# Optimization experiments

Measured on AMD Instinct MI355X. Metric: run time of the kernel, lower is better.

The kernel has to match this reference:

```python
import jax, jax.numpy as jnp
import numpy as np
from jax import lax

TAU = 1.0
LAMBDA_CONTRAST = 1.0
GAMMA_ALIGN = 1.0
EPSILON = 0.1
SINKHORN_ITERS = 50
B, V_EN, V_CN, K, H, D = 512, 30000, 20000, 100, 512, 300


def setup_inputs() -> dict:
    key = jax.random.key(0)
    ks = jax.random.split(key, 24)
    s = lambda fan_in: 1.0 / np.sqrt(fan_in)
    inp = {
        'x_bow_en': jax.random.uniform(ks[0], (B, V_EN), jnp.float32),
        'x_bow_cn': jax.random.uniform(ks[1], (B, V_CN), jnp.float32),
        'cluster_ids': jax.random.randint(ks[2], (B,), 0, 9, jnp.int32),
        'eps_en': jax.random.normal(ks[3], (B, K), jnp.float32),
        'eps_cn': jax.random.normal(ks[4], (B, K), jnp.float32),
        # English encoder params
        'W1_en': jax.random.normal(ks[5], (V_EN, H), jnp.float32) * s(V_EN),
        'b1_en': jnp.zeros((H,), jnp.float32),
        'W2_en': jax.random.normal(ks[6], (H, H), jnp.float32) * s(H),
        'b2_en': jnp.zeros((H,), jnp.float32),
        'Wmu_en': jax.random.normal(ks[7], (H, K), jnp.float32) * s(H),
        'bmu_en': jnp.zeros((K,), jnp.float32),
        'Wlv_en': jax.random.normal(ks[8], (H, K), jnp.float32) * s(H),
        'blv_en': jnp.zeros((K,), jnp.float32),
        # Chinese encoder params
        'W1_cn': jax.random.normal(ks[9], (V_CN, H), jnp.float32) * s(V_CN),
        'b1_cn': jnp.zeros((H,), jnp.float32),
        'W2_cn': jax.random.normal(ks[10], (H, H), jnp.float32) * s(H),
        'b2_cn': jnp.zeros((H,), jnp.float32),
        'Wmu_cn': jax.random.normal(ks[11], (H, K), jnp.float32) * s(H),
        'bmu_cn': jnp.zeros((K,), jnp.float32),
        'Wlv_cn': jax.random.normal(ks[12], (H, K), jnp.float32) * s(H),
        'blv_cn': jnp.zeros((K,), jnp.float32),
        # frozen word embeddings + topic embeddings
        'word_emb_en': jax.random.normal(ks[13], (V_EN, D), jnp.float32),
        'word_emb_cn': jax.random.normal(ks[14], (V_CN, D), jnp.float32),
        'topic_emb': jax.random.normal(ks[15], (K, D), jnp.float32),
    }
    return inp


def _encoder(x, eps, W1, b1, W2, b2, Wmu, bmu, Wlv, blv):
    h = jax.nn.softplus(x @ W1 + b1)
    h = jax.nn.softplus(h @ W2 + b2)
    mu = h @ Wmu + bmu
    logvar = h @ Wlv + blv
    z = mu + eps * jnp.exp(0.5 * logvar)  # reparameterization
    theta = jax.nn.softmax(z, axis=-1)
    return theta, mu, logvar


def _compute_beta(word_emb, topic_emb, tau):
    # torch.cdist p=2 -> euclidean distance [V, K]
    sq = (jnp.sum(word_emb ** 2, -1)[:, None] + jnp.sum(topic_emb ** 2, -1)[None, :]
          - 2.0 * word_emb @ topic_emb.T)
    dist = jnp.sqrt(jnp.maximum(sq, 0.0))
    beta = jnp.exp(-dist / tau)
    beta = beta / jnp.sum(beta, axis=0, keepdims=True)  # normalize over vocab
    return beta.T  # [K, V]


def _tm_loss(x_bow, theta, beta, mu, logvar):
    recon = theta @ beta  # [B, V]
    recon_loss = jnp.mean(-jnp.sum(x_bow * jax.nn.log_softmax(recon, axis=-1), axis=-1))
    kl = jnp.mean(0.5 * jnp.sum(jnp.exp(logvar) + mu ** 2 - 1.0 - logvar, axis=-1))
    return recon_loss + kl


def _contrastive_loss(theta_en, theta_cn, cluster_ids, tau):
    b = theta_en.shape[0]
    parity = (jnp.arange(b) % 2 == 0)[:, None]
    thetas = jnp.where(parity, theta_en, theta_cn)  # anchor/other selection
    tn = thetas / jnp.maximum(jnp.linalg.norm(thetas, axis=-1, keepdims=True), 1e-8)
    E = jnp.exp((tn @ tn.T) / tau)  # exp(cos_sim / tau), [B, B]
    offdiag = ~jnp.eye(b, dtype=bool)
    valid = cluster_ids > 0  # falsy cluster -> skipped, matching torch truthiness
    same = cluster_ids[:, None] == cluster_ids[None, :]
    pos_mask = offdiag & same & valid[:, None] & valid[None, :]
    pos_sim = jnp.sum(jnp.where(pos_mask, E, 0.0), axis=1)
    neg_sum = jnp.sum(jnp.where(offdiag, E, 0.0), axis=1)  # all j != i
    has_pos = valid & (jnp.sum(pos_mask, axis=1) > 0)
    per = -jnp.log(pos_sim / (pos_sim + neg_sum + 1e-8))
    loss = jnp.sum(jnp.where(has_pos, per, 0.0))
    count = jnp.sum(has_pos).astype(jnp.float32)
    return loss / (count + 1e-8)


def _sinkhorn(a, b, C, eps):
    Kmat = jnp.exp(-C / eps)
    def step(uv, _):
        u, v = uv
        u = a / (Kmat @ v + 1e-8)
        v = b / (Kmat.T @ u + 1e-8)
        return (u, v), None
    (u, v), _ = lax.scan(step, (jnp.ones_like(a), jnp.ones_like(b)), None, length=SINKHORN_ITERS)
    return u[:, None] * Kmat * v[None, :]


def _alignment_loss(topic_emb, eps):
    tn = topic_emb / jnp.maximum(jnp.linalg.norm(topic_emb, axis=-1, keepdims=True), 1e-8)
    C = 1.0 - tn @ tn.T
    k = topic_emb.shape[0]
    a = jnp.full((k,), 1.0 / k, jnp.float32)
    Q = _sinkhorn(a, a, C, eps)
    return jnp.sum(Q * C)


def reference(x_bow_en, x_bow_cn, cluster_ids, eps_en, eps_cn,
              W1_en, b1_en, W2_en, b2_en, Wmu_en, bmu_en, Wlv_en, blv_en,
              W1_cn, b1_cn, W2_cn, b2_cn, Wmu_cn, bmu_cn, Wlv_cn, blv_cn,
              word_emb_en, word_emb_cn, topic_emb):
    theta_en, mu_en, lv_en = _encoder(x_bow_en, eps_en, W1_en, b1_en, W2_en, b2_en, Wmu_en, bmu_en, Wlv_en, blv_en)
    theta_cn, mu_cn, lv_cn = _encoder(x_bow_cn, eps_cn, W1_cn, b1_cn, W2_cn, b2_cn, Wmu_cn, bmu_cn, Wlv_cn, blv_cn)
    beta_en = _compute_beta(word_emb_en, topic_emb, TAU)
    beta_cn = _compute_beta(word_emb_cn, topic_emb, TAU)
    tm_en = _tm_loss(x_bow_en, theta_en, beta_en, mu_en, lv_en)
    tm_cn = _tm_loss(x_bow_cn, theta_cn, beta_cn, mu_cn, lv_cn)
    contrast = _contrastive_loss(theta_en, theta_cn, cluster_ids, TAU)
    align = _alignment_loss(topic_emb, EPSILON)
    total = tm_en + tm_cn + LAMBDA_CONTRAST * contrast + GAMMA_ALIGN * align
    return total, tm_en, tm_cn, contrast, align, theta_en, theta_cn, beta_en, beta_cn
```

## Files before the change

kernel.cpp:

```cpp
#include <hip/hip_runtime.h>
#include <math.h>

#define BATCH 512
#define VEN 30000
#define VCN 20000
#define KT 100
#define HID 512
#define DIM 300
#define VENP 30080
#define VCNP 20096
#define KDP 320
#define VENK 30080
#define VCNK 20096

typedef float f32x4 __attribute__((ext_vector_type(4)));
typedef short bf16x8 __attribute__((ext_vector_type(8)));
typedef unsigned short u16x8 __attribute__((ext_vector_type(8)));
typedef unsigned int u32;

#define WS_H1_EN   0
#define WS_H2_EN   (WS_H1_EN + 262144)
#define WS_H1_CN   (WS_H2_EN + 262144)
#define WS_H2_CN   (WS_H1_CN + 262144)
#define WS_ROWS_EN (WS_H2_CN + 262144)
#define WS_ROWS_CN (WS_ROWS_EN + 1536)
#define WS_SCAL    (WS_ROWS_CN + 1536)
#define ZERO_FLOATS (WS_SCAL + 64)
#define WS_BIG     ZERO_FLOATS
#define XB_EN      WS_BIG
#define XB_CN      (WS_BIG + 7700480)
#define WEP_EN     WS_BIG
#define WEP_CN     (WS_BIG + 4812800)
#define TEP        (WS_BIG + 4812800 + 3215360)
#define BT_EN      (WS_BIG + 8048640)
#define BT_CN      (BT_EN + 1925120)
#define THP_EN     (BT_CN + 1286144)
#define THP_CN     (THP_EN + 32768)
#define AFTER_BIG  (WS_BIG + 12845056)
#define W1T_EN     AFTER_BIG
#define W1T_CN     (W1T_EN + 7700480)
#define W2T_EN     (W1T_CN + 5144576)
#define W2T_CN     (W2T_EN + 131072)
#define H1B_EN     (W2T_CN + 131072)
#define H1B_CN     (H1B_EN + 131072)
#define WN2_EN     (H1B_CN + 131072)
#define WN2_CN     (WN2_EN + 30080)
#define TN2        (WN2_CN + 20096)
#define WS_TNBUF   (TN2 + 128)
#define WS_TNT     (WS_TNBUF + 51200)
#define WS_CTOP    (WS_TNT + 30000)
#define WS_COLSUM_EN (WS_CTOP + 10000)
#define WS_COLSUM_CN (WS_COLSUM_EN + 128)

#define OUT_THETA_EN 5
#define OUT_THETA_CN (OUT_THETA_EN + 51200)
#define OUT_BETA_EN  (OUT_THETA_CN + 51200)
#define OUT_BETA_CN  (OUT_BETA_EN + 3000000)

__device__ __forceinline__ float waveReduceSum(float v) {
    #pragma unroll
    for (int o = 32; o > 0; o >>= 1) v += __shfl_down(v, o);
    return v;
}

__device__ __forceinline__ unsigned short f2bf(float f) {
    unsigned int u = __float_as_uint(f);
    u = (u + 0x7FFFu + ((u >> 16) & 1u)) >> 16;
    return (unsigned short)u;
}

__device__ __forceinline__ void gl2lds16(const unsigned short* g, unsigned short* l) {
    __builtin_amdgcn_global_load_lds(
        (const __attribute__((address_space(1))) u32*)g,
        (__attribute__((address_space(3))) u32*)l, 16, 0, 0);
}

__global__ __launch_bounds__(256)
void cast_pad_bf16_kernel(const float* __restrict__ src, unsigned short* __restrict__ dst,
                          int cols, int colsPad)
{
    int row = blockIdx.y;
    int col = (blockIdx.x * 256 + threadIdx.x) * 8;
    if (col >= colsPad) return;
    u16x8 o = {0,0,0,0,0,0,0,0};
    if (col < cols) {
        float4 a = *(const float4*)&src[(size_t)row * cols + col];
        float4 b = *(const float4*)&src[(size_t)row * cols + col + 4];
        o = (u16x8){ f2bf(a.x), f2bf(a.y), f2bf(a.z), f2bf(a.w),
                     f2bf(b.x), f2bf(b.y), f2bf(b.z), f2bf(b.w) };
    }
    *(u16x8*)&dst[(size_t)row * colsPad + col] = o;
}

__global__ __launch_bounds__(256)
void gemm1_async(const unsigned short* __restrict__ A, const unsigned short* __restrict__ B,
                 float* __restrict__ C, int N, int ldA, int ldB, int chunkK, int K)
{
    __shared__ __align__(16) unsigned short As[128 * 64];
    __shared__ __align__(16) unsigned short Bs[128 * 64];
    const int tid = threadIdx.x;
    const int m0 = blockIdx.x * 128, n0 = blockIdx.y * 128;
    const int kStart = blockIdx.z * chunkK;
    const int kEnd = min(kStart + chunkK, K);

    const int wave = tid >> 6, lane = tid & 63;
    const int wm = (wave & 1) * 64, wn = (wave >> 1) * 64;
    const int l15 = lane & 15, quad = lane >> 4;

    const int rl = lane >> 3;
    const int cs = (lane & 7) ^ rl;

    f32x4 acc[4][4];
    #pragma unroll
    for (int i = 0; i < 4; ++i)
        #pragma unroll
        for (int j = 0; j < 4; ++j)
            acc[i][j] = (f32x4){0.f, 0.f, 0.f, 0.f};

    for (int k0 = kStart; k0 < kEnd; k0 += 64) {
        #pragma unroll
        for (int j = 0; j < 4; ++j) {
            int seg = wave * 4 + j;
            int r = seg * 8 + rl;
            gl2lds16(A + (size_t)(m0 + r) * ldA + k0 + cs * 8, &As[seg * 512]);
            gl2lds16(B + (size_t)(n0 + r) * ldB + k0 + cs * 8, &Bs[seg * 512]);
        }
        asm volatile("s_waitcnt vmcnt(0)" ::: "memory");
        __syncthreads();

        #pragma unroll
        for (int kh = 0; kh < 2; ++kh) {
            bf16x8 af[4], bfr[4];
            #pragma unroll
            for (int mi = 0; mi < 4; ++mi) {
                int r = wm + mi * 16 + l15;
                af[mi] = *(const bf16x8*)&As[r * 64 + (((kh << 2) | quad) ^ (r & 7)) * 8];
            }
            #pragma unroll
            for (int ni = 0; ni < 4; ++ni) {
                int r = wn + ni * 16 + l15;
                bfr[ni] = *(const bf16x8*)&Bs[r * 64 + (((kh << 2) | quad) ^ (r & 7)) * 8];
            }
            #pragma unroll
            for (int mi = 0; mi < 4; ++mi)
                #pragma unroll
                for (int ni = 0; ni < 4; ++ni)
                    acc[mi][ni] = __builtin_amdgcn_mfma_f32_16x16x32_bf16(af[mi], bfr[ni], acc[mi][ni], 0, 0, 0);
        }
        __syncthreads();
    }

    #pragma unroll
    for (int mi = 0; mi < 4; ++mi)
        #pragma unroll
        for (int ni = 0; ni < 4; ++ni)
            #pragma unroll
            for (int i = 0; i < 4; ++i) {
                int m = m0 + wm + mi * 16 + quad * 4 + i;
                int n = n0 + wn + ni * 16 + l15;
                atomicAdd(&C[(size_t)m * N + n], acc[mi][ni][i]);
            }
}

template <int MODE, int AF32>
__global__ __launch_bounds__(256)
void mfma_gemm_nt(const void* __restrict__ Av, const unsigned short* __restrict__ B,
                  float* __restrict__ C, int M, int N, int K, int ldA, int ldB, int chunkK,
                  int Mreal, const float* __restrict__ an2, const float* __restrict__ bn2)
{
    __shared__ __align__(16) unsigned short As[128 * 40];
    __shared__ __align__(16) unsigned short Bs[128 * 40];
    const int tid = threadIdx.x;
    const int m0 = blockIdx.x * 128, n0 = blockIdx.y * 128;
    const int kStart = blockIdx.z * chunkK;
    const int kEnd = min(kStart + chunkK, K);

    const int wave = tid >> 6, lane = tid & 63;
    const int wm = (wave & 1) * 64, wn = (wave >> 1) * 64;
    const int l15 = lane & 15, quad = lane >> 4;

    const int srow = tid >> 1;
    const int scol = (tid & 1) * 16;

    f32x4 acc[4][4];
    #pragma unroll
    for (int i = 0; i < 4; ++i)
        #pragma unroll
        for (int j = 0; j < 4; ++j)
            acc[i][j] = (f32x4){0.f, 0.f, 0.f, 0.f};

    const u16x8 z8 = {0,0,0,0,0,0,0,0};

    for (int k0 = kStart; k0 < kEnd; k0 += 32) {
        int kA = k0 + scol;
        if (AF32) {
            const float* pa = (const float*)Av + (size_t)(m0 + srow) * ldA + kA;
            float4 f0 = {0,0,0,0}, f1 = {0,0,0,0}, f2 = {0,0,0,0}, f3 = {0,0,0,0};
            if (kA < kEnd) {
                f0 = *(const float4*)(pa);
                f1 = *(const float4*)(pa + 4);
                f2 = *(const float4*)(pa + 8);
                f3 = *(const float4*)(pa + 12);
            }
            u16x8 o0 = { f2bf(f0.x), f2bf(f0.y), f2bf(f0.z), f2bf(f0.w),
                         f2bf(f1.x), f2bf(f1.y), f2bf(f1.z), f2bf(f1.w) };
            u16x8 o1 = { f2bf(f2.x), f2bf(f2.y), f2bf(f2.z), f2bf(f2.w),
                         f2bf(f3.x), f2bf(f3.y), f2bf(f3.z), f2bf(f3.w) };
            *(u16x8*)&As[srow * 40 + scol]     = o0;
            *(u16x8*)&As[srow * 40 + scol + 8] = o1;
        } else {
            const unsigned short* pa = (const unsigned short*)Av + (size_t)(m0 + srow) * ldA + kA;
            u16x8 a0 = (kA     < kEnd) ? *(const u16x8*)(pa)     : z8;
            u16x8 a1 = (kA + 8 < kEnd) ? *(const u16x8*)(pa + 8) : z8;
            *(u16x8*)&As[srow * 40 + scol]     = a0;
            *(u16x8*)&As[srow * 40 + scol + 8] = a1;
        }
        {
            const unsigned short* pb = B + (size_t)(n0 + srow) * ldB + kA;
            u16x8 b0 = (kA     < kEnd) ? *(const u16x8*)(pb)     : z8;
            u16x8 b1 = (kA + 8 < kEnd) ? *(const u16x8*)(pb + 8) : z8;
            *(u16x8*)&Bs[srow * 40 + scol]     = b0;
            *(u16x8*)&Bs[srow * 40 + scol + 8] = b1;
        }
        __syncthreads();
        bf16x8 af[4], bfr[4];
        #pragma unroll
        for (int mi = 0; mi < 4; ++mi)
            af[mi] = *(const bf16x8*)&As[(wm + mi * 16 + l15) * 40 + quad * 8];
        #pragma unroll
        for (int ni = 0; ni < 4; ++ni)
            bfr[ni] = *(const bf16x8*)&Bs[(wn + ni * 16 + l15) * 40 + quad * 8];
        #pragma unroll
        for (int mi = 0; mi < 4; ++mi)
            #pragma unroll
            for (int ni = 0; ni < 4; ++ni)
                acc[mi][ni] = __builtin_amdgcn_mfma_f32_16x16x32_bf16(af[mi], bfr[ni], acc[mi][ni], 0, 0, 0);
        __syncthreads();
    }

    if (MODE == 0) {
        #pragma unroll
        for (int mi = 0; mi < 4; ++mi)
            #pragma unroll
            for (int ni = 0; ni < 4; ++ni)
                #pragma unroll
                for (int i = 0; i < 4; ++i) {
                    int m = m0 + wm + mi * 16 + quad * 4 + i;
                    int n = n0 + wn + ni * 16 + l15;
                    atomicAdd(&C[(size_t)m * N + n], acc[mi][ni][i]);
                }
    } else {
        #pragma unroll
        for (int mi = 0; mi < 4; ++mi)
            #pragma unroll
            for (int ni = 0; ni < 4; ++ni)
                #pragma unroll
                for (int i = 0; i < 4; ++i) {
                    int m = m0 + wm + mi * 16 + quad * 4 + i;
                    int n = n0 + wn + ni * 16 + l15;
                    if (m < Mreal && n < KT) {
                        float sq = an2[m] + bn2[n] - 2.f * acc[mi][ni][i];
                        C[(size_t)n * Mreal + m] = __expf(-sqrtf(fmaxf(sq, 0.f)));
                    }
                }
    }
}

__global__ __launch_bounds__(256)
void recon_mfma_kernel(const unsigned short* __restrict__ A, const unsigned short* __restrict__ B,
                       const float* __restrict__ x, int V, float* __restrict__ rows)
{
    __shared__ __align__(16) unsigned short As[128 * 40];
    __shared__ __align__(16) unsigned short Bs[128 * 40];
    const int tid = threadIdx.x;
    const int m0 = blockIdx.x * 128, n0 = blockIdx.y * 128;
    const int wave = tid >> 6, lane = tid & 63;
    const int wm = (wave & 1) * 64, wn = (wave >> 1) * 64;
    const int l15 = lane & 15, quad = lane >> 4;
    const int srow = tid >> 1, scol = (tid & 1) * 16;

    f32x4 acc[4][4];
    #pragma unroll
    for (int i = 0; i < 4; ++i)
        #pragma unroll
        for (int j = 0; j < 4; ++j)
            acc[i][j] = (f32x4){0.f, 0.f, 0.f, 0.f};

    for (int k0 = 0; k0 < 128; k0 += 32) {
        int kA = k0 + scol;
        *(u16x8*)&As[srow * 40 + scol]     = *(const u16x8*)(A + (size_t)(m0 + srow) * 128 + kA);
        *(u16x8*)&As[srow * 40 + scol + 8] = *(const u16x8*)(A + (size_t)(m0 + srow) * 128 + kA + 8);
        *(u16x8*)&Bs[srow * 40 + scol]     = *(const u16x8*)(B + (size_t)(n0 + srow) * 128 + kA);
        *(u16x8*)&Bs[srow * 40 + scol + 8] = *(const u16x8*)(B + (size_t)(n0 + srow) * 128 + kA + 8);
        __syncthreads();
        bf16x8 af[4], bfr[4];
        #pragma unroll
        for (int mi = 0; mi < 4; ++mi)
            af[mi] = *(const bf16x8*)&As[(wm + mi * 16 + l15) * 40 + quad * 8];
        #pragma unroll
        for (int ni = 0; ni < 4; ++ni)
            bfr[ni] = *(const bf16x8*)&Bs[(wn + ni * 16 + l15) * 40 + quad * 8];
        #pragma unroll
        for (int mi = 0; mi < 4; ++mi)
            #pragma unroll
            for (int ni = 0; ni < 4; ++ni)
                acc[mi][ni] = __builtin_amdgcn_mfma_f32_16x16x32_bf16(af[mi], bfr[ni], acc[mi][ni], 0, 0, 0);
        __syncthreads();
    }

    #pragma unroll
    for (int ni = 0; ni < 4; ++ni) {
        int b = n0 + wn + ni * 16 + l15;
        float tse = 0.f, tsxr = 0.f, tsx = 0.f;
        #pragma unroll
        for (int mi = 0; mi < 4; ++mi) {
            int v0 = m0 + wm + mi * 16 + quad * 4;
            if (v0 + 3 < V) {
                float4 xv = *(const float4*)&x[(size_t)b * V + v0];
                float xa[4] = {xv.x, xv.y, xv.z, xv.w};
                #pragma unroll
                for (int i = 0; i < 4; ++i) {
                    float r = acc[mi][ni][i];
                    tse += __expf(r);
                    tsxr += xa[i] * r;
                    tsx  += xa[i];
                }
            } else {
                #pragma unroll
                for (int i = 0; i < 4; ++i) {
                    int v = v0 + i;
                    if (v < V) {
                        float xv1 = x[(size_t)b * V + v];
                        float r = acc[mi][ni][i];
                        tse += __expf(r); tsxr += xv1 * r; tsx += xv1;
                    }
                }
            }
        }
        tse  += __shfl_xor(tse, 16);  tse  += __shfl_xor(tse, 32);
        tsxr += __shfl_xor(tsxr, 16); tsxr += __shfl_xor(tsxr, 32);
        tsx  += __shfl_xor(tsx, 16);  tsx  += __shfl_xor(tsx, 32);
        if (quad == 0) {
            atomicAdd(&rows[b], tse);
            atomicAdd(&rows[512 + b], tsxr);
            atomicAdd(&rows[1024 + b], tsx);
        }
    }
}

__global__ __launch_bounds__(256)
void transpose_cast_kernel(const float* __restrict__ src, unsigned short* __restrict__ dst,
                           int K, int N, int Kp)
{
    __shared__ float tile[32][33];
    int kb = blockIdx.x * 32, nb = blockIdx.y * 32;
    int tx = threadIdx.x & 31, ty4 = threadIdx.x >> 5;
    #pragma unroll
    for (int j = 0; j < 4; ++j) {
        int k = kb + ty4 * 4 + j;
        tile[ty4 * 4 + j][tx] = (k < K) ? src[(size_t)k * N + nb + tx] : 0.f;
    }
    __syncthreads();
    #pragma unroll
    for (int j = 0; j < 4; ++j) {
        int n = nb + ty4 * 4 + j;
        int k = kb + tx;
        if (k < Kp) dst[(size_t)n * Kp + k] = f2bf(tile[tx][ty4 * 4 + j]);
    }
}

__global__ void padcast_sqnorm_kernel(const float* __restrict__ src, unsigned short* __restrict__ dst,
                                      float* __restrict__ n2, int V)
{
    int m = blockIdx.x, tid = threadIdx.x;
    float sq = 0.f;
    #pragma unroll
    for (int j = 0; j < 5; ++j) {
        int k = tid + j * 64;
        float v = (m < V && k < DIM) ? src[(size_t)m * DIM + k] : 0.f;
        dst[(size_t)m * KDP + k] = f2bf(v);
        sq += v * v;
    }
    sq = waveReduceSum(sq);
    if (tid == 0) n2[m] = sq;
}

__global__ __launch_bounds__(256)
void normbeta_bt_kernel(float* __restrict__ beta, const float* __restrict__ cs,
                        unsigned short* __restrict__ bt, int V)
{
    int v = blockIdx.x * 64 + (threadIdx.x & 63);
    int kq = threadIdx.x >> 6;
    unsigned short tmp[32];
    #pragma unroll
    for (int j = 0; j < 32; ++j) {
        int k = kq * 32 + j;
        float val = 0.f;
        if (k < KT && v < V) {
            val = beta[(size_t)k * V + v] * (1.0f / cs[k]);
            beta[(size_t)k * V + v] = val;
        }
        tmp[j] = f2bf(val);
    }
    #pragma unroll
    for (int q = 0; q < 4; ++q)
        *(u16x8*)&bt[(size_t)v * 128 + kq * 32 + q * 8] = *(u16x8*)&tmp[q * 8];
}

__global__ void theta_pad_kernel(const float* __restrict__ theta, unsigned short* __restrict__ thp)
{
    int idx = blockIdx.x * 256 + threadIdx.x;
    int b = idx >> 7, k = idx & 127;
    thp[idx] = f2bf(k < KT ? theta[b * KT + k] : 0.f);
}

__global__ __launch_bounds__(256)
void colsum_kernel(const float* __restrict__ bta, float* __restrict__ cs, int V)
{
    int k = blockIdx.x, tid = threadIdx.x;
    float s = 0.f;
    for (int v = tid; v < V; v += 256) s += bta[(size_t)k * V + v];
    s = waveReduceSum(s);
    __shared__ float cw[4];
    if ((tid & 63) == 0) cw[tid >> 6] = s;
    __syncthreads();
    if (tid == 0) cs[k] = cw[0] + cw[1] + cw[2] + cw[3];
}

__global__ void bias_softplus_bf16_kernel(const float* __restrict__ src, const float* __restrict__ b,
                                          unsigned short* __restrict__ dst, int n)
{
    int i = blockIdx.x * 256 + threadIdx.x;
    if (i < n) {
        float x = src[i] + b[i & (HID - 1)];
        float sp = fmaxf(x, 0.f) + log1pf(__expf(-fabsf(x)));
        dst[i] = f2bf(sp);
    }
}

__global__ void bias_softplus_f32_kernel(float* __restrict__ y, const float* __restrict__ b, int n)
{
    int i = blockIdx.x * 256 + threadIdx.x;
    if (i < n) {
        float x = y[i] + b[i & (HID - 1)];
        y[i] = fmaxf(x, 0.f) + log1pf(__expf(-fabsf(x)));
    }
}

__global__ __launch_bounds__(128)
void encoder_head_kernel(const float* __restrict__ h2, const float* __restrict__ Wmu,
                         const float* __restrict__ bmu, const float* __restrict__ Wlv,
                         const float* __restrict__ blv, const float* __restrict__ eps,
                         float* __restrict__ theta_out, float* __restrict__ kl_accum)
{
    int i = blockIdx.x, tid = threadIdx.x;
    __shared__ float hrow[HID];
    __shared__ float sred[128];
    #pragma unroll
    for (int j = 0; j < 4; ++j) hrow[tid + 128 * j] = h2[i * HID + tid + 128 * j];
    __syncthreads();
    float mu = 0.f, lv = 0.f;
    if (tid < KT) {
        #pragma unroll 8
        for (int h = 0; h < HID; ++h) {
            float hv = hrow[h];
            mu += hv * Wmu[h * KT + tid];
            lv += hv * Wlv[h * KT + tid];
        }
        mu += bmu[tid]; lv += blv[tid];
    }
    float z = (tid < KT) ? (mu + eps[i * KT + tid] * __expf(0.5f * lv)) : -3.0e38f;
    sred[tid] = z; __syncthreads();
    for (int s = 64; s > 0; s >>= 1) { if (tid < s) sred[tid] = fmaxf(sred[tid], sred[tid + s]); __syncthreads(); }
    float zmax = sred[0]; __syncthreads();
    float e = (tid < KT) ? __expf(z - zmax) : 0.f;
    sred[tid] = e; __syncthreads();
    for (int s = 64; s > 0; s >>= 1) { if (tid < s) sred[tid] += sred[tid + s]; __syncthreads(); }
    float esum = sred[0]; __syncthreads();
    if (tid < KT) theta_out[i * KT + tid] = e / esum;
    float kterm = (tid < KT) ? 0.5f * (__expf(lv) + mu * mu - 1.f - lv) : 0.f;
    sred[tid] = kterm; __syncthreads();
    for (int s = 64; s > 0; s >>= 1) { if (tid < s) sred[tid] += sred[tid + s]; __syncthreads(); }
    if (tid == 0) atomicAdd(kl_accum, sred[0]);
}

__global__ __launch_bounds__(256)
void recon_finalize_kernel(const float* __restrict__ rows_en, const float* __restrict__ rows_cn,
                           float* __restrict__ scal)
{
    const float* rows = (blockIdx.x == 0) ? rows_en : rows_cn;
    int tid = threadIdx.x;
    float s = 0.f;
    for (int r = tid; r < 512; r += 256) {
        float se = rows[r], sxr = rows[512 + r], sx = rows[1024 + r];
        s += __logf(se) * sx - sxr;
    }
    s = waveReduceSum(s);
    __shared__ float cw[4];
    if ((tid & 63) == 0) cw[tid >> 6] = s;
    __syncthreads();
    if (tid == 0) scal[5 + blockIdx.x] = cw[0] + cw[1] + cw[2] + cw[3];
}

__global__ __launch_bounds__(128)
void contrast_prep_kernel(const float* __restrict__ theta_en, const float* __restrict__ theta_cn,
                          float* __restrict__ tn)
{
    int i = blockIdx.x, tid = threadIdx.x;
    const float* src = ((i & 1) == 0) ? theta_en : theta_cn;
    float val = (tid < KT) ? src[i * KT + tid] : 0.f;
    __shared__ float sred[128];
    sred[tid] = val * val; __syncthreads();
    for (int s = 64; s > 0; s >>= 1) { if (tid < s) sred[tid] += sred[tid + s]; __syncthreads(); }
    float inv = 1.0f / fmaxf(sqrtf(sred[0]), 1e-8f);
    if (tid < KT) tn[i * KT + tid] = val * inv;
}

__global__ __launch_bounds__(256)
void contrast_main_kernel(const float* __restrict__ tn, const int* __restrict__ cid,
                          float* __restrict__ scal)
{
    int i = blockIdx.x, tid = threadIdx.x;
    __shared__ __align__(16) float ti[KT];
    if (tid < KT) ti[tid] = tn[i * KT + tid];
    __syncthreads();
    int ci = cid[i];
    bool vi = ci > 0;
    float pos = 0.f, neg = 0.f, pcnt = 0.f;
    for (int j = tid; j < 512; j += 256) {
        if (j == i) continue;
        float s = 0.f;
        const float4* tj = reinterpret_cast<const float4*>(&tn[j * KT]);
        #pragma unroll
        for (int q = 0; q < 25; ++q) {
            float4 t4 = tj[q];
            s += ti[4 * q] * t4.x + ti[4 * q + 1] * t4.y + ti[4 * q + 2] * t4.z + ti[4 * q + 3] * t4.w;
        }
        float E = __expf(s);
        neg += E;
        if (vi && cid[j] == ci) { pos += E; pcnt += 1.f; }
    }
    pos = waveReduceSum(pos); neg = waveReduceSum(neg); pcnt = waveReduceSum(pcnt);
    __shared__ float cw[3][4];
    int w = tid >> 6;
    if ((tid & 63) == 0) { cw[0][w] = pos; cw[1][w] = neg; cw[2][w] = pcnt; }
    __syncthreads();
    if (tid == 0) {
        float P = 0.f, N = 0.f, PC = 0.f;
        for (int q = 0; q < 4; ++q) { P += cw[0][q]; N += cw[1][q]; PC += cw[2][q]; }
        if (vi && PC > 0.f) {
            atomicAdd(&scal[2], -__logf(P / (P + N + 1e-8f)));
            atomicAdd(&scal[3], 1.0f);
        }
    }
}

__global__ void norm_rows_kernel(const float* __restrict__ A, float* __restrict__ out, int cols)
{
    int r = blockIdx.x, tid = threadIdx.x;
    float s = 0.f;
    for (int d = tid; d < cols; d += 64) { float a = A[r * cols + d]; s += a * a; }
    s = waveReduceSum(s);
    s = __shfl(s, 0);
    float inv = 1.0f / fmaxf(sqrtf(s), 1e-8f);
    for (int d = tid; d < cols; d += 64) out[r * cols + d] = A[r * cols + d] * inv;
}

__global__ __launch_bounds__(128)
void ctopic_kernel(const float* __restrict__ tnt, float* __restrict__ C)
{
    int i = blockIdx.x, tid = threadIdx.x;
    __shared__ float ti[DIM];
    for (int d = tid; d < DIM; d += 128) ti[d] = tnt[i * DIM + d];
    __syncthreads();
    for (int j = tid; j < KT; j += 128) {
        float s = 0.f;
        for (int d = 0; d < DIM; ++d) s += ti[d] * tnt[j * DIM + d];
        C[i * KT + j] = 1.0f - s;
    }
}

__global__ __launch_bounds__(128, 1)
void sinkhorn_kernel(const float* __restrict__ C, float* __restrict__ scal)
{
    __shared__ __align__(16) float ld[100 * 101];
    __shared__ __align__(16) float ub[128], vb[128];
    __shared__ float cw[2];
    const int tid = threadIdx.x;

    for (int i = tid; i < 10000; i += 128) {
        int r = i / 100, c = i - r * 100;
        ld[r * 101 + c] = C[i];
    }
    ub[tid] = 1.f; vb[tid] = 1.f;
    __syncthreads();

    float kr[100], kc[100];
    if (tid < 100) {
        #pragma unroll
        for (int j = 0; j < 100; ++j) kr[j] = __expf(-10.f * ld[tid * 101 + j]);
        #pragma unroll
        for (int j = 0; j < 100; ++j) kc[j] = __expf(-10.f * ld[j * 101 + tid]);
    }

    for (int it = 0; it < 50; ++it) {
        if (tid < 100) {
            float s = 0.f;
            #pragma unroll
            for (int q = 0; q < 25; ++q) {
                float4 v4 = *(const float4*)&vb[q * 4];
                s += kr[q*4]*v4.x + kr[q*4+1]*v4.y + kr[q*4+2]*v4.z + kr[q*4+3]*v4.w;
            }
            ub[tid] = 0.01f / (s + 1e-8f);
        }
        __syncthreads();
        if (tid < 100) {
            float s = 0.f;
            #pragma unroll
            for (int q = 0; q < 25; ++q) {
                float4 u4 = *(const float4*)&ub[q * 4];
                s += kc[q*4]*u4.x + kc[q*4+1]*u4.y + kc[q*4+2]*u4.z + kc[q*4+3]*u4.w;
            }
            vb[tid] = 0.01f / (s + 1e-8f);
        }
        __syncthreads();
    }

    float part = 0.f;
    if (tid < 100) {
        float u = ub[tid];
        #pragma unroll
        for (int q = 0; q < 25; ++q) {
            float4 v4 = *(const float4*)&vb[q * 4];
            float va[4] = {v4.x, v4.y, v4.z, v4.w};
            #pragma unroll
            for (int e = 0; e < 4; ++e) {
                int j = q * 4 + e;
                part += u * kr[j] * va[e] * ld[tid * 101 + j];
            }
        }
    }
    part = waveReduceSum(part);
    if ((tid & 63) == 0) cw[tid >> 6] = part;
    __syncthreads();
    if (tid == 0) scal[4] = cw[0] + cw[1];
}

__global__ void final_combine_kernel(const float* __restrict__ scal, float* __restrict__ out)
{
    if (threadIdx.x == 0 && blockIdx.x == 0) {
        const float invB = 1.0f / 512.0f;
        float tm_en = scal[5] * invB + scal[0] * invB;
        float tm_cn = scal[6] * invB + scal[1] * invB;
        float contrast = scal[2] / (scal[3] + 1e-8f);
        float align = scal[4];
        out[0] = tm_en + tm_cn + contrast + align;
        out[1] = tm_en;
        out[2] = tm_cn;
        out[3] = contrast;
        out[4] = align;
    }
}

extern "C" void kernel_launch(void* const* d_in, const int* in_sizes, int n_in,
                              void* d_out_v, int out_size, void* d_ws, size_t ws_size,
                              hipStream_t stream)
{
    const float* x_en   = (const float*)d_in[0];
    const float* x_cn   = (const float*)d_in[1];
    const int*   cid    = (const int*)  d_in[2];
    const float* eps_en = (const float*)d_in[3];
    const float* eps_cn = (const float*)d_in[4];
    const float* W1_en  = (const float*)d_in[5];
    const float* b1_en  = (const float*)d_in[6];
    const float* W2_en  = (const float*)d_in[7];
    const float* b2_en  = (const float*)d_in[8];
    const float* Wmu_en = (const float*)d_in[9];
    const float* bmu_en = (const float*)d_in[10];
    const float* Wlv_en = (const float*)d_in[11];
    const float* blv_en = (const float*)d_in[12];
    const float* W1_cn  = (const float*)d_in[13];
    const float* b1_cn  = (const float*)d_in[14];
    const float* W2_cn  = (const float*)d_in[15];
    const float* b2_cn  = (const float*)d_in[16];
    const float* Wmu_cn = (const float*)d_in[17];
    const float* bmu_cn = (const float*)d_in[18];
    const float* Wlv_cn = (const float*)d_in[19];
    const float* blv_cn = (const float*)d_in[20];
    const float* we_en  = (const float*)d_in[21];
    const float* we_cn  = (const float*)d_in[22];
    const float* te     = (const float*)d_in[23];
    float* out = (float*)d_out_v;
    float* ws  = (float*)d_ws;

    unsigned short* w1t_en = (unsigned short*)(ws + W1T_EN);
    unsigned short* w1t_cn = (unsigned short*)(ws + W1T_CN);
    unsigned short* w2t_en = (unsigned short*)(ws + W2T_EN);
    unsigned short* w2t_cn = (unsigned short*)(ws + W2T_CN);
    unsigned short* h1b_en = (unsigned short*)(ws + H1B_EN);
    unsigned short* h1b_cn = (unsigned short*)(ws + H1B_CN);
    unsigned short* xb_en  = (unsigned short*)(ws + XB_EN);
    unsigned short* xb_cn  = (unsigned short*)(ws + XB_CN);
    unsigned short* wep_en = (unsigned short*)(ws + WEP_EN);
    unsigned short* wep_cn = (unsigned short*)(ws + WEP_CN);
    unsigned short* tep    = (unsigned short*)(ws + TEP);
    unsigned short* bt_en  = (unsigned short*)(ws + BT_EN);
    unsigned short* bt_cn  = (unsigned short*)(ws + BT_CN);
    unsigned short* thp_en = (unsigned short*)(ws + THP_EN);
    unsigned short* thp_cn = (unsigned short*)(ws + THP_CN);

    hipMemsetAsync(d_ws, 0, (size_t)ZERO_FLOATS * sizeof(float), stream);

    cast_pad_bf16_kernel<<<dim3(15, 512), 256, 0, stream>>>(x_en, xb_en, VEN, VENK);
    cast_pad_bf16_kernel<<<dim3(10, 512), 256, 0, stream>>>(x_cn, xb_cn, VCN, VCNK);

    transpose_cast_kernel<<<dim3(940, 16), 256, 0, stream>>>(W1_en, w1t_en, VEN, HID, VENK);
    transpose_cast_kernel<<<dim3(628, 16), 256, 0, stream>>>(W1_cn, w1t_cn, VCN, HID, VCNK);
    transpose_cast_kernel<<<dim3(16, 16), 256, 0, stream>>>(W2_en, w2t_en, HID, HID, HID);
    transpose_cast_kernel<<<dim3(16, 16), 256, 0, stream>>>(W2_cn, w2t_cn, HID, HID, HID);

    gemm1_async<<<dim3(4, 4, 47), 256, 0, stream>>>(xb_en, w1t_en, ws + WS_H1_EN,
        HID, VENK, VENK, 640, VENK);
    gemm1_async<<<dim3(4, 4, 32), 256, 0, stream>>>(xb_cn, w1t_cn, ws + WS_H1_CN,
        HID, VCNK, VCNK, 640, VCNK);

    bias_softplus_bf16_kernel<<<1024, 256, 0, stream>>>(ws + WS_H1_EN, b1_en, h1b_en, 262144);
    bias_softplus_bf16_kernel<<<1024, 256, 0, stream>>>(ws + WS_H1_CN, b1_cn, h1b_cn, 262144);

    mfma_gemm_nt<0, 0><<<dim3(4, 4, 16), 256, 0, stream>>>(h1b_en, w2t_en, ws + WS_H2_EN,
        BATCH, HID, HID, HID, HID, 32, 0, nullptr, nullptr);
    mfma_gemm_nt<0, 0><<<dim3(4, 4, 16), 256, 0, stream>>>(h1b_cn, w2t_cn, ws + WS_H2_CN,
        BATCH, HID, HID, HID, HID, 32, 0, nullptr, nullptr);

    bias_softplus_f32_kernel<<<1024, 256, 0, stream>>>(ws + WS_H2_EN, b2_en, 262144);
    bias_softplus_f32_kernel<<<1024, 256, 0, stream>>>(ws + WS_H2_CN, b2_cn, 262144);

    encoder_head_kernel<<<BATCH, 128, 0, stream>>>(ws + WS_H2_EN, Wmu_en, bmu_en, Wlv_en, blv_en,
                                                   eps_en, out + OUT_THETA_EN, ws + WS_SCAL + 0);
    encoder_head_kernel<<<BATCH, 128, 0, stream>>>(ws + WS_H2_CN, Wmu_cn, bmu_cn, Wlv_cn, blv_cn,
                                                   eps_cn, out + OUT_THETA_CN, ws + WS_SCAL + 1);

    padcast_sqnorm_kernel<<<VENP, 64, 0, stream>>>(we_en, wep_en, ws + WN2_EN, VEN);
    padcast_sqnorm_kernel<<<VCNP, 64, 0, stream>>>(we_cn, wep_cn, ws + WN2_CN, VCN);
    padcast_sqnorm_kernel<<<128, 64, 0, stream>>>(te, tep, ws + TN2, KT);

    mfma_gemm_nt<2, 0><<<dim3(235, 1, 1), 256, 0, stream>>>(wep_en, tep, out + OUT_BETA_EN,
        VENP, 128, KDP, KDP, KDP, KDP, VEN, ws + WN2_EN, ws + TN2);
    mfma_gemm_nt<2, 0><<<dim3(157, 1, 1), 256, 0, stream>>>(wep_cn, tep, out + OUT_BETA_CN,
        VCNP, 128, KDP, KDP, KDP, KDP, VCN, ws + WN2_CN, ws + TN2);

    colsum_kernel<<<KT, 256, 0, stream>>>(out + OUT_BETA_EN, ws + WS_COLSUM_EN, VEN);
    colsum_kernel<<<KT, 256, 0, stream>>>(out + OUT_BETA_CN, ws + WS_COLSUM_CN, VCN);

    normbeta_bt_kernel<<<VENP / 64, 256, 0, stream>>>(out + OUT_BETA_EN, ws + WS_COLSUM_EN, bt_en, VEN);
    normbeta_bt_kernel<<<VCNP / 64, 256, 0, stream>>>(out + OUT_BETA_CN, ws + WS_COLSUM_CN, bt_cn, VCN);

    theta_pad_kernel<<<256, 256, 0, stream>>>(out + OUT_THETA_EN, thp_en);
    theta_pad_kernel<<<256, 256, 0, stream>>>(out + OUT_THETA_CN, thp_cn);

    recon_mfma_kernel<<<dim3(VENP / 128, 4), 256, 0, stream>>>(bt_en, thp_en, x_en, VEN, ws + WS_ROWS_EN);
    recon_mfma_kernel<<<dim3(VCNP / 128, 4), 256, 0, stream>>>(bt_cn, thp_cn, x_cn, VCN, ws + WS_ROWS_CN);
    recon_finalize_kernel<<<2, 256, 0, stream>>>(ws + WS_ROWS_EN, ws + WS_ROWS_CN, ws + WS_SCAL);

    contrast_prep_kernel<<<BATCH, 128, 0, stream>>>(out + OUT_THETA_EN, out + OUT_THETA_CN, ws + WS_TNBUF);
    contrast_main_kernel<<<BATCH, 256, 0, stream>>>(ws + WS_TNBUF, cid, ws + WS_SCAL);

    norm_rows_kernel<<<KT, 64, 0, stream>>>(te, ws + WS_TNT, DIM);
    ctopic_kernel<<<KT, 128, 0, stream>>>(ws + WS_TNT, ws + WS_CTOP);
    sinkhorn_kernel<<<1, 128, 0, stream>>>(ws + WS_CTOP, ws + WS_SCAL);

    final_combine_kernel<<<1, 64, 0, stream>>>(ws + WS_SCAL, out);
}
```

Measured before the change: 891.2 us.

## Unify GEMMs on async LDS loader, drop split-K for layer 2, split Sinkhorn threads

```diff
diff --git a/kernel.cpp b/kernel.cpp
--- a/kernel.cpp
+++ b/kernel.cpp
@@ -92,9 +92,11 @@
     *(u16x8*)&dst[(size_t)row * colsPad + col] = o;
 }
 
-__global__ __launch_bounds__(256)
-void gemm1_async(const unsigned short* __restrict__ A, const unsigned short* __restrict__ B,
-                 float* __restrict__ C, int N, int ldA, int ldB, int chunkK, int K)
+template <int MODE>
+__global__ __launch_bounds__(256)
+void gemm_async(const unsigned short* __restrict__ A, const unsigned short* __restrict__ B,
+                float* __restrict__ C, int N, int ldA, int ldB, int chunkK, int K,
+                int Mreal, const float* __restrict__ an2, const float* __restrict__ bn2)
 {
     __shared__ __align__(16) unsigned short As[128 * 64];
     __shared__ __align__(16) unsigned short Bs[128 * 64];
@@ -158,126 +160,32 @@
             for (int i = 0; i < 4; ++i) {
                 int m = m0 + wm + mi * 16 + quad * 4 + i;
                 int n = n0 + wn + ni * 16 + l15;
-                atomicAdd(&C[(size_t)m * N + n], acc[mi][ni][i]);
-            }
-}
-
-template <int MODE, int AF32>
-__global__ __launch_bounds__(256)
-void mfma_gemm_nt(const void* __restrict__ Av, const unsigned short* __restrict__ B,
-                  float* __restrict__ C, int M, int N, int K, int ldA, int ldB, int chunkK,
-                  int Mreal, const float* __restrict__ an2, const float* __restrict__ bn2)
-{
-    __shared__ __align__(16) unsigned short As[128 * 40];
-    __shared__ __align__(16) unsigned short Bs[128 * 40];
-    const int tid = threadIdx.x;
-    const int m0 = blockIdx.x * 128, n0 = blockIdx.y * 128;
-    const int kStart = blockIdx.z * chunkK;
-    const int kEnd = min(kStart + chunkK, K);
-
-    const int wave = tid >> 6, lane = tid & 63;
-    const int wm = (wave & 1) * 64, wn = (wave >> 1) * 64;
-    const int l15 = lane & 15, quad = lane >> 4;
-
-    const int srow = tid >> 1;
-    const int scol = (tid & 1) * 16;
-
-    f32x4 acc[4][4];
-    #pragma unroll
-    for (int i = 0; i < 4; ++i)
-        #pragma unroll
-        for (int j = 0; j < 4; ++j)
-            acc[i][j] = (f32x4){0.f, 0.f, 0.f, 0.f};
-
-    const u16x8 z8 = {0,0,0,0,0,0,0,0};
-
-    for (int k0 = kStart; k0 < kEnd; k0 += 32) {
-        int kA = k0 + scol;
-        if (AF32) {
-            const float* pa = (const float*)Av + (size_t)(m0 + srow) * ldA + kA;
-            float4 f0 = {0,0,0,0}, f1 = {0,0,0,0}, f2 = {0,0,0,0}, f3 = {0,0,0,0};
-            if (kA < kEnd) {
-                f0 = *(const float4*)(pa);
-                f1 = *(const float4*)(pa + 4);
-                f2 = *(const float4*)(pa + 8);
-                f3 = *(const float4*)(pa + 12);
-            }
-            u16x8 o0 = { f2bf(f0.x), f2bf(f0.y), f2bf(f0.z), f2bf(f0.w),
-                         f2bf(f1.x), f2bf(f1.y), f2bf(f1.z), f2bf(f1.w) };
-            u16x8 o1 = { f2bf(f2.x), f2bf(f2.y), f2bf(f2.z), f2bf(f2.w),
-                         f2bf(f3.x), f2bf(f3.y), f2bf(f3.z), f2bf(f3.w) };
-            *(u16x8*)&As[srow * 40 + scol]     = o0;
-            *(u16x8*)&As[srow * 40 + scol + 8] = o1;
-        } else {
-            const unsigned short* pa = (const unsigned short*)Av + (size_t)(m0 + srow) * ldA + kA;
-            u16x8 a0 = (kA     < kEnd) ? *(const u16x8*)(pa)     : z8;
-            u16x8 a1 = (kA + 8 < kEnd) ? *(const u16x8*)(pa + 8) : z8;
-            *(u16x8*)&As[srow * 40 + scol]     = a0;
-            *(u16x8*)&As[srow * 40 + scol + 8] = a1;
-        }
-        {
-            const unsigned short* pb = B + (size_t)(n0 + srow) * ldB + kA;
-            u16x8 b0 = (kA     < kEnd) ? *(const u16x8*)(pb)     : z8;
-            u16x8 b1 = (kA + 8 < kEnd) ? *(const u16x8*)(pb + 8) : z8;
-            *(u16x8*)&Bs[srow * 40 + scol]     = b0;
-            *(u16x8*)&Bs[srow * 40 + scol + 8] = b1;
-        }
-        __syncthreads();
-        bf16x8 af[4], bfr[4];
-        #pragma unroll
-        for (int mi = 0; mi < 4; ++mi)
-            af[mi] = *(const bf16x8*)&As[(wm + mi * 16 + l15) * 40 + quad * 8];
-        #pragma unroll
-        for (int ni = 0; ni < 4; ++ni)
-            bfr[ni] = *(const bf16x8*)&Bs[(wn + ni * 16 + l15) * 40 + quad * 8];
-        #pragma unroll
-        for (int mi = 0; mi < 4; ++mi)
-            #pragma unroll
-            for (int ni = 0; ni < 4; ++ni)
-                acc[mi][ni] = __builtin_amdgcn_mfma_f32_16x16x32_bf16(af[mi], bfr[ni], acc[mi][ni], 0, 0, 0);
-        __syncthreads();
-    }
-
-    if (MODE == 0) {
-        #pragma unroll
-        for (int mi = 0; mi < 4; ++mi)
-            #pragma unroll
-            for (int ni = 0; ni < 4; ++ni)
-                #pragma unroll
-                for (int i = 0; i < 4; ++i) {
-                    int m = m0 + wm + mi * 16 + quad * 4 + i;
-                    int n = n0 + wn + ni * 16 + l15;
+                if (MODE == 0) {
                     atomicAdd(&C[(size_t)m * N + n], acc[mi][ni][i]);
-                }
-    } else {
-        #pragma unroll
-        for (int mi = 0; mi < 4; ++mi)
-            #pragma unroll
-            for (int ni = 0; ni < 4; ++ni)
-                #pragma unroll
-                for (int i = 0; i < 4; ++i) {
-                    int m = m0 + wm + mi * 16 + quad * 4 + i;
-                    int n = n0 + wn + ni * 16 + l15;
+                } else if (MODE == 1) {
+                    C[(size_t)m * N + n] = acc[mi][ni][i];
+                } else {
                     if (m < Mreal && n < KT) {
                         float sq = an2[m] + bn2[n] - 2.f * acc[mi][ni][i];
                         C[(size_t)n * Mreal + m] = __expf(-sqrtf(fmaxf(sq, 0.f)));
                     }
                 }
-    }
+            }
 }
 
 __global__ __launch_bounds__(256)
 void recon_mfma_kernel(const unsigned short* __restrict__ A, const unsigned short* __restrict__ B,
                        const float* __restrict__ x, int V, float* __restrict__ rows)
 {
-    __shared__ __align__(16) unsigned short As[128 * 40];
-    __shared__ __align__(16) unsigned short Bs[128 * 40];
+    __shared__ __align__(16) unsigned short As[128 * 64];
+    __shared__ __align__(16) unsigned short Bs[128 * 64];
     const int tid = threadIdx.x;
     const int m0 = blockIdx.x * 128, n0 = blockIdx.y * 128;
     const int wave = tid >> 6, lane = tid & 63;
     const int wm = (wave & 1) * 64, wn = (wave >> 1) * 64;
     const int l15 = lane & 15, quad = lane >> 4;
-    const int srow = tid >> 1, scol = (tid & 1) * 16;
+    const int rl = lane >> 3;
+    const int cs = (lane & 7) ^ rl;
 
     f32x4 acc[4][4];
     #pragma unroll
@@ -286,25 +194,36 @@
         for (int j = 0; j < 4; ++j)
             acc[i][j] = (f32x4){0.f, 0.f, 0.f, 0.f};
 
-    for (int k0 = 0; k0 < 128; k0 += 32) {
-        int kA = k0 + scol;
-        *(u16x8*)&As[srow * 40 + scol]     = *(const u16x8*)(A + (size_t)(m0 + srow) * 128 + kA);
-        *(u16x8*)&As[srow * 40 + scol + 8] = *(const u16x8*)(A + (size_t)(m0 + srow) * 128 + kA + 8);
-        *(u16x8*)&Bs[srow * 40 + scol]     = *(const u16x8*)(B + (size_t)(n0 + srow) * 128 + kA);
-        *(u16x8*)&Bs[srow * 40 + scol + 8] = *(const u16x8*)(B + (size_t)(n0 + srow) * 128 + kA + 8);
+    for (int k0 = 0; k0 < 128; k0 += 64) {
+        #pragma unroll
+        for (int j = 0; j < 4; ++j) {
+            int seg = wave * 4 + j;
+            int r = seg * 8 + rl;
+            gl2lds16(A + (size_t)(m0 + r) * 128 + k0 + cs * 8, &As[seg * 512]);
+            gl2lds16(B + (size_t)(n0 + r) * 128 + k0 + cs * 8, &Bs[seg * 512]);
+        }
+        asm volatile("s_waitcnt vmcnt(0)" ::: "memory");
         __syncthreads();
-        bf16x8 af[4], bfr[4];
-        #pragma unroll
-        for (int mi = 0; mi < 4; ++mi)
-            af[mi] = *(const bf16x8*)&As[(wm + mi * 16 + l15) * 40 + quad * 8];
-        #pragma unroll
-        for (int ni = 0; ni < 4; ++ni)
-            bfr[ni] = *(const bf16x8*)&Bs[(wn + ni * 16 + l15) * 40 + quad * 8];
-        #pragma unroll
-        for (int mi = 0; mi < 4; ++mi)
-            #pragma unroll
-            for (int ni = 0; ni < 4; ++ni)
-                acc[mi][ni] = __builtin_amdgcn_mfma_f32_16x16x32_bf16(af[mi], bfr[ni], acc[mi][ni], 0, 0, 0);
+
+        #pragma unroll
+        for (int kh = 0; kh < 2; ++kh) {
+            bf16x8 af[4], bfr[4];
+            #pragma unroll
+            for (int mi = 0; mi < 4; ++mi) {
+                int r = wm + mi * 16 + l15;
+                af[mi] = *(const bf16x8*)&As[r * 64 + (((kh << 2) | quad) ^ (r & 7)) * 8];
+            }
+            #pragma unroll
+            for (int ni = 0; ni < 4; ++ni) {
+                int r = wn + ni * 16 + l15;
+                bfr[ni] = *(const bf16x8*)&Bs[r * 64 + (((kh << 2) | quad) ^ (r & 7)) * 8];
+            }
+            #pragma unroll
+            for (int mi = 0; mi < 4; ++mi)
+                #pragma unroll
+                for (int ni = 0; ni < 4; ++ni)
+                    acc[mi][ni] = __builtin_amdgcn_mfma_f32_16x16x32_bf16(af[mi], bfr[ni], acc[mi][ni], 0, 0, 0);
+        }
         __syncthreads();
     }
 
@@ -580,70 +499,63 @@
     }
 }
 
-__global__ __launch_bounds__(128, 1)
+__global__ __launch_bounds__(256, 1)
 void sinkhorn_kernel(const float* __restrict__ C, float* __restrict__ scal)
 {
-    __shared__ __align__(16) float ld[100 * 101];
     __shared__ __align__(16) float ub[128], vb[128];
-    __shared__ float cw[2];
+    __shared__ float cw[4];
     const int tid = threadIdx.x;
-
-    for (int i = tid; i < 10000; i += 128) {
-        int r = i / 100, c = i - r * 100;
-        ld[r * 101 + c] = C[i];
-    }
-    ub[tid] = 1.f; vb[tid] = 1.f;
-    __syncthreads();
-
-    float kr[100], kc[100];
-    if (tid < 100) {
-        #pragma unroll
-        for (int j = 0; j < 100; ++j) kr[j] = __expf(-10.f * ld[tid * 101 + j]);
-        #pragma unroll
-        for (int j = 0; j < 100; ++j) kc[j] = __expf(-10.f * ld[j * 101 + tid]);
-    }
+    const bool gA = (tid < 100);
+    const bool gB = (tid >= 128 && tid < 228);
+    const int rc = gA ? tid : (tid - 128);
+
+    float kk[100];
+    if (gA) {
+        #pragma unroll
+        for (int j = 0; j < 100; ++j) kk[j] = __expf(-10.f * C[rc * 100 + j]);
+    } else if (gB) {
+        #pragma unroll
+        for (int j = 0; j < 100; ++j) kk[j] = __expf(-10.f * C[j * 100 + rc]);
+    }
+    if (tid < 128) { ub[tid] = 1.f; vb[tid] = 1.f; }
+    __syncthreads();
 
     for (int it = 0; it < 50; ++it) {
-        if (tid < 100) {
+        if (gA) {
             float s = 0.f;
             #pragma unroll
             for (int q = 0; q < 25; ++q) {
                 float4 v4 = *(const float4*)&vb[q * 4];
-                s += kr[q*4]*v4.x + kr[q*4+1]*v4.y + kr[q*4+2]*v4.z + kr[q*4+3]*v4.w;
-            }
-            ub[tid] = 0.01f / (s + 1e-8f);
+                s += kk[q*4]*v4.x + kk[q*4+1]*v4.y + kk[q*4+2]*v4.z + kk[q*4+3]*v4.w;
+            }
+            ub[rc] = 0.01f / (s + 1e-8f);
         }
         __syncthreads();
-        if (tid < 100) {
+        if (gB) {
             float s = 0.f;
             #pragma unroll
             for (int q = 0; q < 25; ++q) {
                 float4 u4 = *(const float4*)&ub[q * 4];
-                s += kc[q*4]*u4.x + kc[q*4+1]*u4.y + kc[q*4+2]*u4.z + kc[q*4+3]*u4.w;
-            }
-            vb[tid] = 0.01f / (s + 1e-8f);
+                s += kk[q*4]*u4.x + kk[q*4+1]*u4.y + kk[q*4+2]*u4.z + kk[q*4+3]*u4.w;
+            }
+            vb[rc] = 0.01f / (s + 1e-8f);
         }
         __syncthreads();
     }
 
     float part = 0.f;
-    if (tid < 100) {
-        float u = ub[tid];
-        #pragma unroll
-        for (int q = 0; q < 25; ++q) {
-            float4 v4 = *(const float4*)&vb[q * 4];
-            float va[4] = {v4.x, v4.y, v4.z, v4.w};
-            #pragma unroll
-            for (int e = 0; e < 4; ++e) {
-                int j = q * 4 + e;
-                part += u * kr[j] * va[e] * ld[tid * 101 + j];
-            }
+    if (gA) {
+        float u = ub[rc];
+        #pragma unroll
+        for (int j = 0; j < 100; ++j) {
+            float k = kk[j];
+            part += u * k * vb[j] * (-0.1f * __logf(k));
         }
     }
     part = waveReduceSum(part);
     if ((tid & 63) == 0) cw[tid >> 6] = part;
     __syncthreads();
-    if (tid == 0) scal[4] = cw[0] + cw[1];
+    if (tid == 0) scal[4] = cw[0] + cw[1] + cw[2] + cw[3];
 }
 
 __global__ void final_combine_kernel(const float* __restrict__ scal, float* __restrict__ out)
@@ -719,18 +631,18 @@
     transpose_cast_kernel<<<dim3(16, 16), 256, 0, stream>>>(W2_en, w2t_en, HID, HID, HID);
     transpose_cast_kernel<<<dim3(16, 16), 256, 0, stream>>>(W2_cn, w2t_cn, HID, HID, HID);
 
-    gemm1_async<<<dim3(4, 4, 47), 256, 0, stream>>>(xb_en, w1t_en, ws + WS_H1_EN,
-        HID, VENK, VENK, 640, VENK);
-    gemm1_async<<<dim3(4, 4, 32), 256, 0, stream>>>(xb_cn, w1t_cn, ws + WS_H1_CN,
-        HID, VCNK, VCNK, 640, VCNK);
+    gemm_async<0><<<dim3(4, 4, 47), 256, 0, stream>>>(xb_en, w1t_en, ws + WS_H1_EN,
+        HID, VENK, VENK, 640, VENK, 0, nullptr, nullptr);
+    gemm_async<0><<<dim3(4, 4, 32), 256, 0, stream>>>(xb_cn, w1t_cn, ws + WS_H1_CN,
+        HID, VCNK, VCNK, 640, VCNK, 0, nullptr, nullptr);
 
     bias_softplus_bf16_kernel<<<1024, 256, 0, stream>>>(ws + WS_H1_EN, b1_en, h1b_en, 262144);
     bias_softplus_bf16_kernel<<<1024, 256, 0, stream>>>(ws + WS_H1_CN, b1_cn, h1b_cn, 262144);
 
-    mfma_gemm_nt<0, 0><<<dim3(4, 4, 16), 256, 0, stream>>>(h1b_en, w2t_en, ws + WS_H2_EN,
-        BATCH, HID, HID, HID, HID, 32, 0, nullptr, nullptr);
-    mfma_gemm_nt<0, 0><<<dim3(4, 4, 16), 256, 0, stream>>>(h1b_cn, w2t_cn, ws + WS_H2_CN,
-        BATCH, HID, HID, HID, HID, 32, 0, nullptr, nullptr);
+    gemm_async<1><<<dim3(4, 4, 1), 256, 0, stream>>>(h1b_en, w2t_en, ws + WS_H2_EN,
+        HID, HID, HID, HID, HID, 0, nullptr, nullptr);
+    gemm_async<1><<<dim3(4, 4, 1), 256, 0, stream>>>(h1b_cn, w2t_cn, ws + WS_H2_CN,
+        HID, HID, HID, HID, HID, 0, nullptr, nullptr);
 
     bias_softplus_f32_kernel<<<1024, 256, 0, stream>>>(ws + WS_H2_EN, b2_en, 262144);
     bias_softplus_f32_kernel<<<1024, 256, 0, stream>>>(ws + WS_H2_CN, b2_cn, 262144);
@@ -744,10 +656,10 @@
     padcast_sqnorm_kernel<<<VCNP, 64, 0, stream>>>(we_cn, wep_cn, ws + WN2_CN, VCN);
     padcast_sqnorm_kernel<<<128, 64, 0, stream>>>(te, tep, ws + TN2, KT);
 
-    mfma_gemm_nt<2, 0><<<dim3(235, 1, 1), 256, 0, stream>>>(wep_en, tep, out + OUT_BETA_EN,
-        VENP, 128, KDP, KDP, KDP, KDP, VEN, ws + WN2_EN, ws + TN2);
-    mfma_gemm_nt<2, 0><<<dim3(157, 1, 1), 256, 0, stream>>>(wep_cn, tep, out + OUT_BETA_CN,
-        VCNP, 128, KDP, KDP, KDP, KDP, VCN, ws + WN2_CN, ws + TN2);
+    gemm_async<2><<<dim3(235, 1, 1), 256, 0, stream>>>(wep_en, tep, out + OUT_BETA_EN,
+        128, KDP, KDP, KDP, KDP, VEN, ws + WN2_EN, ws + TN2);
+    gemm_async<2><<<dim3(157, 1, 1), 256, 0, stream>>>(wep_cn, tep, out + OUT_BETA_CN,
+        128, KDP, KDP, KDP, KDP, VCN, ws + WN2_CN, ws + TN2);
 
     colsum_kernel<<<KT, 256, 0, stream>>>(out + OUT_BETA_EN, ws + WS_COLSUM_EN, VEN);
     colsum_kernel<<<KT, 256, 0, stream>>>(out + OUT_BETA_CN, ws + WS_COLSUM_CN, VCN);
@@ -767,7 +679,7 @@
 
     norm_rows_kernel<<<KT, 64, 0, stream>>>(te, ws + WS_TNT, DIM);
     ctopic_kernel<<<KT, 128, 0, stream>>>(ws + WS_TNT, ws + WS_CTOP);
-    sinkhorn_kernel<<<1, 128, 0, stream>>>(ws + WS_CTOP, ws + WS_SCAL);
+    sinkhorn_kernel<<<1, 256, 0, stream>>>(ws + WS_CTOP, ws + WS_SCAL);
 
     final_combine_kernel<<<1, 64, 0, stream>>>(ws + WS_SCAL, out);
 }
```

New measurement: 887.7 us. About the same (-0.4%).
